# Optimization experiments

Hardware: AMD Instinct MI355X
Metric: run time of the kernel (lower is better)

The kernel has to match this reference:

```python
import jax, jax.numpy as jnp
import numpy as np

N_EMBD = 1024  # scale uses C**-0.5 with C = n_embd, as in the original code


def setup_inputs() -> dict:
    key = jax.random.key(0)
    k1, k2, k3, k4 = jax.random.split(key, 4)
    B, T, C, H = 4, 2048, N_EMBD, 64
    x = jax.random.normal(k1, (B, T, C), dtype=jnp.float32)
    # torch Linear weight is [out,in]; we store transposed [in,out] and scale like default init
    s = 1.0 / np.sqrt(C)
    Wq = jax.random.normal(k2, (C, H), dtype=jnp.float32) * s
    Wk = jax.random.normal(k3, (C, H), dtype=jnp.float32) * s
    Wv = jax.random.normal(k4, (C, H), dtype=jnp.float32) * s
    return {"x": x, "Wq": Wq, "Wk": Wk, "Wv": Wv}


def reference(x, Wq, Wk, Wv):
    B, T, C = x.shape
    q = jnp.einsum('btc,ch->bth', x, Wq)
    k = jnp.einsum('btc,ch->bth', x, Wk)
    v = jnp.einsum('btc,ch->bth', x, Wv)
    # kv_cache is None: k,v are the new cache; full causal mask
    scale = C ** -0.5  # NOTE: original scales by n_embd, not head_size
    wei = jnp.einsum('bqh,bkh->bqk', q, k) * scale  # [B,T,T]
    causal = jnp.tril(jnp.ones((T, T), dtype=bool))
    wei = jnp.where(causal, wei, -jnp.inf)
    wei = jax.nn.softmax(wei, axis=-1)
    # dropout: identity (eval mode / deterministic reference)
    out = jnp.einsum('bqk,bkh->bqh', wei, v)
    return (out, k, v)
```

## Files before the change

### kernel.cpp

```cpp
#include <hip/hip_runtime.h>
#include <hip/hip_bf16.h>
#include <stdint.h>


#define NB 4
#define TT 2048
#define CC 1024
#define HH 64
#define NKV (NB * TT * HH)

typedef __attribute__((ext_vector_type(8))) short short8;
typedef __attribute__((ext_vector_type(4))) float f32x4;

__device__ __forceinline__ unsigned short f2bf(float f) {
    union { float f; unsigned int i; } v;
    v.f = f;
    unsigned int r = v.i + 0x7fffu + ((v.i >> 16) & 1u);
    return (unsigned short)(r >> 16);
}
__device__ __forceinline__ unsigned int pkbf2(float a, float b) {
    __hip_bfloat162 h = __float22bfloat162_rn(make_float2(a, b));
    union { __hip_bfloat162 h; unsigned int u; } c;
    c.h = h;
    return c.u;
}

__global__ __launch_bounds__(256) void prep_wb(const float* __restrict__ Wq,
                                               const float* __restrict__ Wk,
                                               const float* __restrict__ Wv,
                                               unsigned short* __restrict__ Wb) {
    int gid = blockIdx.x * 256 + threadIdx.x;
    int j  = gid & 7;
    int l  = (gid >> 3) & 63;
    int kk = (gid >> 9) & 31;
    int s  = gid >> 14;
    int k  = kk * 32 + (l >> 4) * 8 + j;
    int h  = (s & 3) * 16 + (l & 15);
    const float* W = (s >> 2) == 0 ? Wq : (s >> 2) == 1 ? Wk : Wv;
    Wb[gid] = f2bf(W[(size_t)k * HH + h]);
}

#define XSTR 1032
#define SC2F 0.0450842200113808f

__global__ __launch_bounds__(256) void qkv_mfma(const float* __restrict__ x,
                                                const unsigned short* __restrict__ Wb,
                                                float* __restrict__ out,
                                                unsigned short* __restrict__ qb,
                                                unsigned short* __restrict__ kb,
                                                unsigned short* __restrict__ vT) {
    __shared__ __align__(16) unsigned short xs[16 * XSTR];
    const int t    = threadIdx.x;
    const int wave = t >> 6, lane = t & 63;
    const int n    = lane & 15, quad = lane >> 4;
    const int row0 = blockIdx.x * 16;
    const int b    = row0 >> 11;

#pragma unroll 8
    for (int i = 0; i < 16; ++i) {
        float4 f = *(const float4*)(x + (size_t)(row0 + i) * CC + 4 * t);
        uint2 u;
        u.x = pkbf2(f.x, f.y);
        u.y = pkbf2(f.z, f.w);
        *(uint2*)&xs[i * XSTR + 4 * t] = u;
    }
    __syncthreads();

    f32x4 acc0 = (f32x4){0.f, 0.f, 0.f, 0.f};
    f32x4 acc1 = acc0, acc2 = acc0;

    const unsigned short* wp = Wb + (size_t)lane * 8;
    const size_t fs = (size_t)32 * 64 * 8;

#pragma unroll 4
    for (int kk = 0; kk < 32; ++kk) {
        short8 a = *(const short8*)&xs[n * XSTR + kk * 32 + quad * 8];
        const unsigned short* wk_ = wp + (size_t)kk * 512;
        short8 b0 = *(const short8*)(wk_ + (size_t)(wave)     * fs);
        short8 b1 = *(const short8*)(wk_ + (size_t)(wave + 4) * fs);
        short8 b2 = *(const short8*)(wk_ + (size_t)(wave + 8) * fs);
        acc0 = __builtin_amdgcn_mfma_f32_16x16x32_bf16(a, b0, acc0, 0, 0, 0);
        acc1 = __builtin_amdgcn_mfma_f32_16x16x32_bf16(a, b1, acc1, 0, 0, 0);
        acc2 = __builtin_amdgcn_mfma_f32_16x16x32_bf16(a, b2, acc2, 0, 0, 0);
    }

    const int h = wave * 16 + n;
    const size_t g0 = (size_t)(row0 + quad * 4) * HH + h;

    unsigned int uq01 = pkbf2(acc0[0] * SC2F, acc0[1] * SC2F);
    unsigned int uq23 = pkbf2(acc0[2] * SC2F, acc0[3] * SC2F);
    unsigned int uk01 = pkbf2(acc1[0], acc1[1]);
    unsigned int uk23 = pkbf2(acc1[2], acc1[3]);
    qb[g0]          = (unsigned short)uq01;
    qb[g0 + HH]     = (unsigned short)(uq01 >> 16);
    qb[g0 + 2 * HH] = (unsigned short)uq23;
    qb[g0 + 3 * HH] = (unsigned short)(uq23 >> 16);
    kb[g0]          = (unsigned short)uk01;
    kb[g0 + HH]     = (unsigned short)(uk01 >> 16);
    kb[g0 + 2 * HH] = (unsigned short)uk23;
    kb[g0 + 3 * HH] = (unsigned short)(uk23 >> 16);
#pragma unroll
    for (int r = 0; r < 4; ++r) {
        out[NKV + g0 + (size_t)r * HH]     = acc1[r];
        out[2 * NKV + g0 + (size_t)r * HH] = acc2[r];
    }
    uint2 uv;
    uv.x = pkbf2(acc2[0], acc2[1]);
    uv.y = pkbf2(acc2[2], acc2[3]);
    *(uint2*)&vT[(size_t)(b * HH + h) * TT + (row0 & 2047) + quad * 4] = uv;
}

__global__ __launch_bounds__(256) void attn_mfma(float* __restrict__ out,
                                                 const unsigned short* __restrict__ qb,
                                                 const unsigned short* __restrict__ kb,
                                                 const unsigned short* __restrict__ vT) {
    __shared__ __align__(16) unsigned short Ps[4][16][72];
    __shared__ float Lb[4][64][4];
    __shared__ float Ob[4][64][16];

    const int t    = threadIdx.x;
    const int wave = t >> 6, lane = t & 63;
    const int n    = lane & 15, quad = lane >> 4;
    const int b    = blockIdx.y;
    const int qt   = (b < 2) ? blockIdx.x : 127 - blockIdx.x;
    const int q0   = qt * 16;

    const unsigned short* qr = qb + (size_t)(b * TT + q0 + n) * HH + quad * 8;
    short8 aq0 = *(const short8*)(qr);
    short8 aq1 = *(const short8*)(qr + 32);

    f32x4 oc[4];
#pragma unroll
    for (int d = 0; d < 4; ++d) oc[d] = (f32x4){0.f, 0.f, 0.f, 0.f};
    float l_[4] = {0.f, 0.f, 0.f, 0.f};

    const int nkt = (q0 >> 6) + 1;

    for (int kt = wave; kt < nkt; kt += 4) {
        const int j0 = kt * 64;

        short8 bk0[4], bk1[4];
#pragma unroll
        for (int s = 0; s < 4; ++s) {
            const unsigned short* kr = kb + (size_t)(b * TT + j0 + s * 16 + n) * HH + quad * 8;
            bk0[s] = *(const short8*)(kr);
            bk1[s] = *(const short8*)(kr + 32);
        }

        short8 bv0[4], bv1[4];
#pragma unroll
        for (int d = 0; d < 4; ++d) {
            const unsigned short* vr = vT + (size_t)(b * HH + d * 16 + n) * TT + j0 + quad * 8;
            bv0[d] = *(const short8*)(vr);
            bv1[d] = *(const short8*)(vr + 32);
        }

        f32x4 sc[4];
#pragma unroll
        for (int s = 0; s < 4; ++s) sc[s] = (f32x4){0.f, 0.f, 0.f, 0.f};
        __builtin_amdgcn_s_setprio(1);
#pragma unroll
        for (int s = 0; s < 4; ++s) {
            sc[s] = __builtin_amdgcn_mfma_f32_16x16x32_bf16(aq0, bk0[s], sc[s], 0, 0, 0);
            sc[s] = __builtin_amdgcn_mfma_f32_16x16x32_bf16(aq1, bk1[s], sc[s], 0, 0, 0);
        }
        __builtin_amdgcn_s_setprio(0);

        float p[4][4];
        if (j0 + 63 <= q0) {
#pragma unroll
            for (int s = 0; s < 4; ++s)
#pragma unroll
                for (int r = 0; r < 4; ++r) {
                    float pe = exp2f(sc[s][r]);
                    p[s][r] = pe;
                    l_[r] += pe;
                }
        } else {
#pragma unroll
            for (int r = 0; r < 4; ++r) {
                const int qrow = q0 + quad * 4 + r;
#pragma unroll
                for (int s = 0; s < 4; ++s) {
                    int krow = j0 + s * 16 + n;
                    float pe = (krow <= qrow) ? exp2f(sc[s][r]) : 0.f;
                    p[s][r] = pe;
                    l_[r] += pe;
                }
            }
        }

#pragma unroll
        for (int s = 0; s < 4; ++s) {
            unsigned int u01 = pkbf2(p[s][0], p[s][1]);
            unsigned int u23 = pkbf2(p[s][2], p[s][3]);
            Ps[wave][quad * 4 + 0][s * 16 + n] = (unsigned short)u01;
            Ps[wave][quad * 4 + 1][s * 16 + n] = (unsigned short)(u01 >> 16);
            Ps[wave][quad * 4 + 2][s * 16 + n] = (unsigned short)u23;
            Ps[wave][quad * 4 + 3][s * 16 + n] = (unsigned short)(u23 >> 16);
        }
        __asm__ volatile("s_waitcnt lgkmcnt(0)" ::: "memory");
        short8 ap0 = *(const short8*)&Ps[wave][n][quad * 8];
        short8 ap1 = *(const short8*)&Ps[wave][n][32 + quad * 8];

        __builtin_amdgcn_s_setprio(1);
#pragma unroll
        for (int d = 0; d < 4; ++d) {
            oc[d] = __builtin_amdgcn_mfma_f32_16x16x32_bf16(ap0, bv0[d], oc[d], 0, 0, 0);
            oc[d] = __builtin_amdgcn_mfma_f32_16x16x32_bf16(ap1, bv1[d], oc[d], 0, 0, 0);
        }
        __builtin_amdgcn_s_setprio(0);
    }

#pragma unroll
    for (int off = 1; off < 16; off <<= 1)
#pragma unroll
        for (int r = 0; r < 4; ++r)
            l_[r] += __shfl_xor(l_[r], off);

#pragma unroll
    for (int r = 0; r < 4; ++r) Lb[wave][lane][r] = l_[r];
#pragma unroll
    for (int d = 0; d < 4; ++d)
#pragma unroll
        for (int r = 0; r < 4; ++r)
            Ob[wave][lane][d * 4 + r] = oc[d][r];
    __syncthreads();

    if (wave == 0) {
#pragma unroll
        for (int r = 0; r < 4; ++r) {
            float ls = Lb[0][lane][r] + Lb[1][lane][r] + Lb[2][lane][r] + Lb[3][lane][r];
            const float inv = 1.f / ls;
#pragma unroll
            for (int d = 0; d < 4; ++d) {
                float o = Ob[0][lane][d * 4 + r] + Ob[1][lane][d * 4 + r] +
                          Ob[2][lane][d * 4 + r] + Ob[3][lane][d * 4 + r];
                out[(size_t)(b * TT + q0 + quad * 4 + r) * HH + d * 16 + n] = o * inv;
            }
        }
    }
}

extern "C" void kernel_launch(void* const* d_in, const int* in_sizes, int n_in,
                              void* d_out, int out_size, void* d_ws, size_t ws_size,
                              hipStream_t stream) {
    const float* x  = (const float*)d_in[0];
    const float* Wq = (const float*)d_in[1];
    const float* Wk = (const float*)d_in[2];
    const float* Wv = (const float*)d_in[3];
    float* out = (float*)d_out;

    char* ws = (char*)d_ws;
    unsigned short* Wb = (unsigned short*)(ws);
    unsigned short* qb = (unsigned short*)(ws + (1u << 20));
    unsigned short* kb = (unsigned short*)(ws + (2u << 20));
    unsigned short* vT = (unsigned short*)(ws + (3u << 20));

    prep_wb<<<768, 256, 0, stream>>>(Wq, Wk, Wv, Wb);
    qkv_mfma<<<512, 256, 0, stream>>>(x, Wb, out, qb, kb, vT);
    attn_mfma<<<dim3(128, 4), 256, 0, stream>>>(out, qb, kb, vT);
}
```

Before: 107.4 us.

## Pair complementary causal query tiles per block with proportional wave split

Each attention block now handles two query tiles, qt and 127-qt, using 8 waves. The waves are split between the two tiles in proportion to their causal key-tile counts, and each group reduces and writes its own output. This is meant to even out the causal-mask load across blocks, where the old code only reversed the tile order for some batches. The cost is a bigger block with more shared memory, half as many blocks, and rounding in the wave split that can leave a group underused.

```diff
diff --git a/kernel.cpp b/kernel.cpp
--- a/kernel.cpp
+++ b/kernel.cpp
@@ -110,20 +110,32 @@
     *(uint2*)&vT[(size_t)(b * HH + h) * TT + (row0 & 2047) + quad * 4] = uv;
 }
 
-__global__ __launch_bounds__(256) void attn_mfma(float* __restrict__ out,
+__global__ __launch_bounds__(512) void attn_mfma(float* __restrict__ out,
                                                  const unsigned short* __restrict__ qb,
                                                  const unsigned short* __restrict__ kb,
                                                  const unsigned short* __restrict__ vT) {
-    __shared__ __align__(16) unsigned short Ps[4][16][72];
-    __shared__ float Lb[4][64][4];
-    __shared__ float Ob[4][64][16];
+    __shared__ __align__(16) unsigned short Ps[8][16][72];
+    __shared__ float Lb[8][64][4];
+    __shared__ float Ob[8][64][16];
 
     const int t    = threadIdx.x;
     const int wave = t >> 6, lane = t & 63;
     const int n    = lane & 15, quad = lane >> 4;
     const int b    = blockIdx.y;
-    const int qt   = (b < 2) ? blockIdx.x : 127 - blockIdx.x;
-    const int q0   = qt * 16;
+
+    const int qtA = blockIdx.x;
+    const int qtB = 127 - blockIdx.x;
+    const int nA  = (qtA >> 2) + 1;
+    const int nB  = (qtB >> 2) + 1;
+    int wA = (8 * nA + 16) / 33;
+    wA = wA < 1 ? 1 : (wA > 7 ? 7 : wA);
+
+    const int inA     = (wave < wA);
+    const int qt      = inA ? qtA : qtB;
+    const int kt0     = inA ? wave : wave - wA;
+    const int kstride = inA ? wA : 8 - wA;
+    const int nkt     = inA ? nA : nB;
+    const int q0      = qt * 16;
 
     const unsigned short* qr = qb + (size_t)(b * TT + q0 + n) * HH + quad * 8;
     short8 aq0 = *(const short8*)(qr);
@@ -134,9 +146,7 @@
     for (int d = 0; d < 4; ++d) oc[d] = (f32x4){0.f, 0.f, 0.f, 0.f};
     float l_[4] = {0.f, 0.f, 0.f, 0.f};
 
-    const int nkt = (q0 >> 6) + 1;
-
-    for (int kt = wave; kt < nkt; kt += 4) {
+    for (int kt = kt0; kt < nkt; kt += kstride) {
         const int j0 = kt * 64;
 
         short8 bk0[4], bk1[4];
@@ -227,16 +237,21 @@
             Ob[wave][lane][d * 4 + r] = oc[d][r];
     __syncthreads();
 
-    if (wave == 0) {
+    if (wave == 0 || wave == wA) {
+        const int w0 = (wave == 0) ? 0 : wA;
+        const int w1 = (wave == 0) ? wA : 8;
+        const int qm = (wave == 0) ? qtA : qtB;
+        const int qb0 = qm * 16;
 #pragma unroll
         for (int r = 0; r < 4; ++r) {
-            float ls = Lb[0][lane][r] + Lb[1][lane][r] + Lb[2][lane][r] + Lb[3][lane][r];
+            float ls = 0.f;
+            for (int w = w0; w < w1; ++w) ls += Lb[w][lane][r];
             const float inv = 1.f / ls;
 #pragma unroll
             for (int d = 0; d < 4; ++d) {
-                float o = Ob[0][lane][d * 4 + r] + Ob[1][lane][d * 4 + r] +
-                          Ob[2][lane][d * 4 + r] + Ob[3][lane][d * 4 + r];
-                out[(size_t)(b * TT + q0 + quad * 4 + r) * HH + d * 16 + n] = o * inv;
+                float o = 0.f;
+                for (int w = w0; w < w1; ++w) o += Ob[w][lane][d * 4 + r];
+                out[(size_t)(b * TT + qb0 + quad * 4 + r) * HH + d * 16 + n] = o * inv;
             }
         }
     }
@@ -259,5 +274,5 @@
 
     prep_wb<<<768, 256, 0, stream>>>(Wq, Wk, Wv, Wb);
     qkv_mfma<<<512, 256, 0, stream>>>(x, Wb, out, qb, kb, vT);
-    attn_mfma<<<dim3(128, 4), 256, 0, stream>>>(out, qb, kb, vT);
-}
+    attn_mfma<<<dim3(64, 4), 512, 0, stream>>>(out, qb, kb, vT);
+}
```

Result: slower. 114.1 us (+6.3%).

## Double QKV projection row tile per block and swizzle LDS x layout

Applied to the files above, without the earlier changes.

The QKV projection kernel now handles 32 rows per block with 512 threads: two groups of four waves each take 16 rows and share the same weight fragment indices, so weight fetches per block are reused across twice as many rows. The padded LDS stride is replaced by an XOR swizzle on the 1024-wide row to avoid bank conflicts without padding. The grid is halved to 256 blocks, which lowers parallelism across CUs and uses 64KB of LDS per block.

```diff
diff --git a/kernel.cpp b/kernel.cpp
--- a/kernel.cpp
+++ b/kernel.cpp
@@ -40,29 +40,33 @@
     Wb[gid] = f2bf(W[(size_t)k * HH + h]);
 }
 
-#define XSTR 1032
 #define SC2F 0.0450842200113808f
 
-__global__ __launch_bounds__(256) void qkv_mfma(const float* __restrict__ x,
+__global__ __launch_bounds__(512) void qkv_mfma(const float* __restrict__ x,
                                                 const unsigned short* __restrict__ Wb,
                                                 float* __restrict__ out,
                                                 unsigned short* __restrict__ qb,
                                                 unsigned short* __restrict__ kb,
                                                 unsigned short* __restrict__ vT) {
-    __shared__ __align__(16) unsigned short xs[16 * XSTR];
+    __shared__ __align__(16) unsigned short xs[32 * 1024];
     const int t    = threadIdx.x;
     const int wave = t >> 6, lane = t & 63;
     const int n    = lane & 15, quad = lane >> 4;
-    const int row0 = blockIdx.x * 16;
+    const int fw   = wave & 3, rt = wave >> 2;
+    const int row0 = blockIdx.x * 32;
     const int b    = row0 >> 11;
 
+    {
+        const int tr = t >> 8, tc = t & 255;
 #pragma unroll 8
-    for (int i = 0; i < 16; ++i) {
-        float4 f = *(const float4*)(x + (size_t)(row0 + i) * CC + 4 * t);
-        uint2 u;
-        u.x = pkbf2(f.x, f.y);
-        u.y = pkbf2(f.z, f.w);
-        *(uint2*)&xs[i * XSTR + 4 * t] = u;
+        for (int it = 0; it < 16; ++it) {
+            const int i = it * 2 + tr;
+            float4 f = *(const float4*)(x + (size_t)(row0 + i) * CC + 4 * tc);
+            uint2 u;
+            u.x = pkbf2(f.x, f.y);
+            u.y = pkbf2(f.z, f.w);
+            *(uint2*)&xs[i * 1024 + ((tc ^ ((i & 7) << 1)) << 2)] = u;
+        }
     }
     __syncthreads();
 
@@ -71,21 +75,23 @@
 
     const unsigned short* wp = Wb + (size_t)lane * 8;
     const size_t fs = (size_t)32 * 64 * 8;
+    const int arow = (rt * 16 + n) * 1024;
+    const int axor = (n & 7) << 1;
 
 #pragma unroll 4
     for (int kk = 0; kk < 32; ++kk) {
-        short8 a = *(const short8*)&xs[n * XSTR + kk * 32 + quad * 8];
+        short8 a = *(const short8*)&xs[arow + (((kk * 8 + quad * 2) ^ axor) << 2)];
         const unsigned short* wk_ = wp + (size_t)kk * 512;
-        short8 b0 = *(const short8*)(wk_ + (size_t)(wave)     * fs);
-        short8 b1 = *(const short8*)(wk_ + (size_t)(wave + 4) * fs);
-        short8 b2 = *(const short8*)(wk_ + (size_t)(wave + 8) * fs);
+        short8 b0 = *(const short8*)(wk_ + (size_t)(fw)     * fs);
+        short8 b1 = *(const short8*)(wk_ + (size_t)(fw + 4) * fs);
+        short8 b2 = *(const short8*)(wk_ + (size_t)(fw + 8) * fs);
         acc0 = __builtin_amdgcn_mfma_f32_16x16x32_bf16(a, b0, acc0, 0, 0, 0);
         acc1 = __builtin_amdgcn_mfma_f32_16x16x32_bf16(a, b1, acc1, 0, 0, 0);
         acc2 = __builtin_amdgcn_mfma_f32_16x16x32_bf16(a, b2, acc2, 0, 0, 0);
     }
 
-    const int h = wave * 16 + n;
-    const size_t g0 = (size_t)(row0 + quad * 4) * HH + h;
+    const int h = fw * 16 + n;
+    const size_t g0 = (size_t)(row0 + rt * 16 + quad * 4) * HH + h;
 
     unsigned int uq01 = pkbf2(acc0[0] * SC2F, acc0[1] * SC2F);
     unsigned int uq23 = pkbf2(acc0[2] * SC2F, acc0[3] * SC2F);
@@ -107,7 +113,7 @@
     uint2 uv;
     uv.x = pkbf2(acc2[0], acc2[1]);
     uv.y = pkbf2(acc2[2], acc2[3]);
-    *(uint2*)&vT[(size_t)(b * HH + h) * TT + (row0 & 2047) + quad * 4] = uv;
+    *(uint2*)&vT[(size_t)(b * HH + h) * TT + ((row0 + rt * 16) & 2047) + quad * 4] = uv;
 }
 
 __global__ __launch_bounds__(256) void attn_mfma(float* __restrict__ out,
@@ -258,6 +264,6 @@
     unsigned short* vT = (unsigned short*)(ws + (3u << 20));
 
     prep_wb<<<768, 256, 0, stream>>>(Wq, Wk, Wv, Wb);
-    qkv_mfma<<<512, 256, 0, stream>>>(x, Wb, out, qb, kb, vT);
+    qkv_mfma<<<256, 512, 0, stream>>>(x, Wb, out, qb, kb, vT);
     attn_mfma<<<dim3(128, 4), 256, 0, stream>>>(out, qb, kb, vT);
 }
```

New measurement: 106.9 us. Within noise of the previous version (-0.4%).
